# Performance work log

Hardware: AMD Instinct MI355X
Metric: run time of the kernel (lower is better)

The kernel has to match this reference:

```python
import jax, jax.numpy as jnp
import numpy as np
from jax import lax

T, B, D, H, C, G = 32, 512, 1024, 2048, 10, 16
BETA = 0.95
THRESH = 1.0


def _build_mask(key, out_f, in_f, p_intra=1.0, p_inter=0.15):
    ig, og = in_f // G, out_f // G
    same = (jnp.arange(out_f) // og)[:, None] == (jnp.arange(in_f) // ig)[None, :]
    probs = jnp.where(same, p_intra, p_inter)
    return (jax.random.uniform(key, (out_f, in_f)) < probs).astype(jnp.float32)


def setup_inputs() -> dict:
    key = jax.random.key(0)
    ks = jax.random.split(key, 12)
    def w(k, out_f, in_f):
        return jax.random.normal(k, (out_f, in_f), jnp.float32) * (1.0 / np.sqrt(in_f))
    return {
        'x_seq': jax.random.normal(ks[0], (T, B, D), jnp.float32),
        'w1': w(ks[1], H, D), 'b1': jax.random.normal(ks[2], (H,), jnp.float32) * 0.01,
        'mask1': _build_mask(ks[3], H, D),
        'w2': w(ks[4], H, H), 'b2': jax.random.normal(ks[5], (H,), jnp.float32) * 0.01,
        'mask2': _build_mask(ks[6], H, H),
        'w3': w(ks[7], H, H), 'b3': jax.random.normal(ks[8], (H,), jnp.float32) * 0.01,
        'mask3': _build_mask(ks[9], H, H),
        'w_out': w(ks[10], C, H), 'b_out': jax.random.normal(ks[11], (C,), jnp.float32) * 0.01,
    }


@jax.custom_vjp
def spike(x):
    # heaviside fire, fast_sigmoid(slope=25) surrogate gradient
    return (x > 0).astype(x.dtype)

def _spike_fwd(x):
    return spike(x), x

def _spike_bwd(x, g):
    return (g / (25.0 * jnp.abs(x) + 1.0) ** 2,)

spike.defvjp(_spike_fwd, _spike_bwd)


def _lif(cur, mem):
    # snntorch Leaky (reset-by-subtraction): reset from previous mem (detached)
    reset = lax.stop_gradient((mem > THRESH).astype(cur.dtype))
    mem = BETA * mem + cur - reset * THRESH
    spk = spike(mem - THRESH)
    return spk, mem


def reference(x_seq, w1, b1, mask1, w2, b2, mask2, w3, b3, mask3, w_out, b_out):
    # cache masked weights once (same math as per-step weight*mask)
    ew1, ew2, ew3 = w1 * mask1, w2 * mask2, w3 * mask3
    Bsz = x_seq.shape[1]
    mem1 = jnp.zeros((Bsz, H), x_seq.dtype)
    mem2 = jnp.zeros((Bsz, H), x_seq.dtype)
    mem3 = jnp.zeros((Bsz, H), x_seq.dtype)
    mem_o = jnp.zeros((Bsz, C), x_seq.dtype)
    ssum = jnp.zeros((Bsz, C), x_seq.dtype)

    def step(carry, x_t):
        mem1, mem2, mem3, mem_o, ssum = carry
        spk1, mem1 = _lif(x_t @ ew1.T + b1, mem1)
        spk2, mem2 = _lif(spk1 @ ew2.T + b2, mem2)
        spk3, mem3 = _lif(spk2 @ ew3.T + b3, mem3)
        spk_o, mem_o = _lif(spk3 @ w_out.T + b_out, mem_o)
        return (mem1, mem2, mem3, mem_o, ssum + spk_o), None

    (mem1, mem2, mem3, mem_o, ssum), _ = lax.scan(step, (mem1, mem2, mem3, mem_o, ssum), x_seq)
    return ssum
```

## Files before the change

kernel.cpp:

```cpp
#include <hip/hip_runtime.h>

#define TSTEPS 32
#define BSZ    512
#define DIN    1024
#define HID    2048
#define NCLS   10
#define BETA   0.95f
#define VTH    1.0f
#define SPKB   ((size_t)BSZ * (HID / 8))

typedef __attribute__((ext_vector_type(4))) float          f4;
typedef __attribute__((ext_vector_type(4))) float          f32x4;
typedef __attribute__((ext_vector_type(8))) __bf16         bf16x8;
typedef __attribute__((ext_vector_type(8))) unsigned short us8;
typedef __attribute__((ext_vector_type(4))) unsigned short us4;
typedef __attribute__((ext_vector_type(2))) unsigned int   u32x2;

__device__ inline unsigned short f2bf(float f) {
    unsigned u = __float_as_uint(f);
    u += 0x7FFF + ((u >> 16) & 1);
    return (unsigned short)(u >> 16);
}
__device__ inline float bf2f(unsigned short h) {
    return __uint_as_float(((unsigned)h) << 16);
}

__device__ __forceinline__ void split_f4pair(f4 v0, f4 v1, us8& o0, us8& o1, us8& o2) {
#pragma unroll
    for (int jj = 0; jj < 4; jj++) {
        float v = v0[jj];
        unsigned short h1 = f2bf(v); float r = v - bf2f(h1);
        unsigned short h2 = f2bf(r); float r2 = r - bf2f(h2);
        o0[jj] = h1; o1[jj] = h2; o2[jj] = f2bf(r2);
        v = v1[jj];
        h1 = f2bf(v); r = v - bf2f(h1);
        h2 = f2bf(r); r2 = r - bf2f(h2);
        o0[jj + 4] = h1; o1[jj + 4] = h2; o2[jj + 4] = f2bf(r2);
    }
}

__global__ __launch_bounds__(256)
void split3(const float* __restrict__ w, const float* __restrict__ m,
            unsigned short* __restrict__ h1, unsigned short* __restrict__ h2,
            unsigned short* __restrict__ h3, int n4)
{
    int i      = blockIdx.x * blockDim.x + threadIdx.x;
    int stride = gridDim.x * blockDim.x;
    for (; i < n4; i += stride) {
        f4 wv = ((const f4*)w)[i];
        f4 mv = ((const f4*)m)[i];
        us4 a, b, c;
#pragma unroll
        for (int j = 0; j < 4; j++) {
            float e  = wv[j] * mv[j];
            unsigned short x1 = f2bf(e);
            float r  = e - bf2f(x1);
            unsigned short x2 = f2bf(r);
            float r2 = r - bf2f(x2);
            a[j] = x1; b[j] = x2; c[j] = f2bf(r2);
        }
        ((us4*)h1)[i] = a;
        ((us4*)h2)[i] = b;
        ((us4*)h3)[i] = c;
    }
}

__global__ __launch_bounds__(256)
void split3q(const float* __restrict__ w, const float* __restrict__ m,
             unsigned short* __restrict__ q)
{
    const int NK = HID * HID;
    int gid = blockIdx.x * 256 + threadIdx.x;
    const int lane = gid & 63;
    const int t    = gid >> 6;
    const int kt   = t & (HID / 32 - 1);
    const int nt   = t >> 6;
    const int n = nt * 16 + (lane & 15);
    const int k = kt * 32 + (lane >> 4) * 8;
    const size_t src = (size_t)n * HID + k;
    f4 w0 = *(const f4*)(w + src),     w1v = *(const f4*)(w + src + 4);
    f4 m0 = *(const f4*)(m + src),     m1v = *(const f4*)(m + src + 4);
    us8 q0, q1, q2;
    split_f4pair(w0 * m0, w1v * m1v, q0, q1, q2);
    ((us8*)q)[gid]            = q0;
    ((us8*)(q + NK))[gid]     = q1;
    ((us8*)(q + 2 * NK))[gid] = q2;
}

__global__ __launch_bounds__(256)
void zerof(float* __restrict__ p, int n4)
{
    int i      = blockIdx.x * blockDim.x + threadIdx.x;
    int stride = gridDim.x * blockDim.x;
    f4 z = {0.f, 0.f, 0.f, 0.f};
    for (; i < n4; i += stride) ((f4*)p)[i] = z;
}

__device__ __forceinline__ void xsplit_dev(const float* __restrict__ xt,
                                           unsigned short* __restrict__ dst,
                                           int bid, int nblk, int tid)
{
    const int n4 = BSZ * DIN / 4;
    const int PS = BSZ * DIN;
    int i      = bid * 256 + tid;
    int stride = nblk * 256;
    for (; i < n4; i += stride) {
        f4 v = ((const f4*)xt)[i];
        us4 a, b, c;
#pragma unroll
        for (int j = 0; j < 4; j++) {
            float e = v[j];
            unsigned short x1 = f2bf(e);
            float r  = e - bf2f(x1);
            unsigned short x2 = f2bf(r);
            float r2 = r - bf2f(x2);
            a[j] = x1; b[j] = x2; c[j] = f2bf(r2);
        }
        ((us4*)(dst))[i]          = a;
        ((us4*)(dst + PS))[i]     = b;
        ((us4*)(dst + 2 * PS))[i] = c;
    }
}

__global__ __launch_bounds__(256)
void xsplit_k(const float* __restrict__ xt, unsigned short* __restrict__ dst)
{
    xsplit_dev(xt, dst, blockIdx.x, gridDim.x, threadIdx.x);
}

__device__ __forceinline__ void lif_epi(const f32x4 acc[2][2], const float* __restrict__ bias,
                                        float* __restrict__ memOut, unsigned char* __restrict__ sbits,
                                        int bm, int bn, int wm, int wn, int lane)
{
    const int fr = lane & 15;
#pragma unroll
    for (int fm = 0; fm < 2; fm++)
#pragma unroll
        for (int fn = 0; fn < 2; fn++) {
            const int n  = bn * 64 + wn * 32 + fn * 16 + fr;
            const float bv = bias[n];
            const int rbase = bm * 64 + wm * 32 + fm * 16 + (lane >> 4) * 4;
#pragma unroll
            for (int r = 0; r < 4; r++) {
                const int row = rbase + r;
                float* mp = memOut + (size_t)row * HID + n;
                float mo  = *mp;
                float m2  = BETA * mo + (acc[fm][fn][r] + bv) - ((mo > VTH) ? VTH : 0.f);
                *mp = m2;
                unsigned long long bal = __ballot(m2 > VTH);
                if (fr == 0) {
                    unsigned short bits = (unsigned short)(bal >> ((lane >> 4) * 16));
                    *(unsigned short*)(sbits + (size_t)row * (HID / 8) + bn * 8 + wn * 4 + fn * 2) = bits;
                }
            }
        }
}

__device__ __forceinline__ void lif_epi4b(const f32x4 (&acc)[4], const float* __restrict__ bias,
                                          float* __restrict__ memOut,
                                          unsigned char* __restrict__ sbitsOut,
                                          int bm, int bn, int wv, int lane)
{
    const int fr = lane & 15;
    const int n  = bn * 64 + wv * 16 + fr;
    const float bv = bias[n];
#pragma unroll
    for (int fm = 0; fm < 4; fm++) {
        const int rbase = bm * 64 + fm * 16 + (lane >> 4) * 4;
#pragma unroll
        for (int r = 0; r < 4; r++) {
            const int row = rbase + r;
            float* mp = memOut + (size_t)row * HID + n;
            float mo  = *mp;
            float m2  = BETA * mo + (acc[fm][r] + bv) - ((mo > VTH) ? VTH : 0.f);
            *mp = m2;
            unsigned long long bal = __ballot(m2 > VTH);
            if (fr == 0) {
                unsigned short bits = (unsigned short)(bal >> ((lane >> 4) * 16));
                *(unsigned short*)(sbitsOut + (size_t)row * (HID / 8) + bn * 8 + wv * 2) = bits;
            }
        }
    }
}

__device__ __forceinline__ void role_out_b(const unsigned char* __restrict__ sbits,
    const float* __restrict__ wo, const float* __restrict__ bo,
    float* __restrict__ memo, float* __restrict__ ssum, int b, int lane)
{
    const unsigned int bits = *(const unsigned int*)(sbits + (size_t)b * (HID / 8) + lane * 4);
    float acc[NCLS];
#pragma unroll
    for (int c = 0; c < NCLS; c++) {
        const f4* wrow = (const f4*)(wo + (size_t)c * HID + lane * 32);
        float s = 0.f;
#pragma unroll
        for (int q = 0; q < 8; q++) {
            f4 w = wrow[q];
#pragma unroll
            for (int i = 0; i < 4; i++)
                if ((bits >> (q * 4 + i)) & 1u) s += w[i];
        }
        acc[c] = s;
    }
#pragma unroll
    for (int c = 0; c < NCLS; c++)
#pragma unroll
        for (int m = 1; m < 64; m <<= 1) acc[c] += __shfl_xor(acc[c], m, 64);

    if (lane == 0) {
#pragma unroll
        for (int c = 0; c < NCLS; c++) {
            float mo  = memo[b * NCLS + c];
            float rst = (mo > VTH) ? VTH : 0.f;
            float m2  = BETA * mo + acc[c] + bo[c] - rst;
            memo[b * NCLS + c] = m2;
            if (m2 > VTH) ssum[b * NCLS + c] += 1.f;
        }
    }
}

__device__ __forceinline__ void role_l23k(unsigned char* smem,
    const unsigned char* __restrict__ sbitsIn,
    const unsigned short* __restrict__ Bq,
    const float* __restrict__ bias, float* __restrict__ memOut,
    unsigned char* __restrict__ sbitsOut, int rb, int tid)
{
    u32x2* lut = (u32x2*)smem;
    if (tid < 16) {
        u32x2 e;
        e.x = ((tid & 1) ? 0x3F80u : 0u) | ((tid & 2) ? 0x3F800000u : 0u);
        e.y = ((tid & 4) ? 0x3F80u : 0u) | ((tid & 8) ? 0x3F800000u : 0u);
        lut[tid] = e;
    }
    __syncthreads();

    const int bn = rb & 31, bm = rb >> 5;
    const int lane = tid & 63, wv = tid >> 6;
    const int fr = lane & 15, fk = (lane >> 4) * 8;

    const size_t PSQ = (size_t)HID * HID / 8;
    const us8* bP0 = (const us8*)Bq + (size_t)(bn * 4 + wv) * (HID / 32) * 64 + lane;
    const us8* bP1 = bP0 + PSQ;
    const us8* bP2 = bP1 + PSQ;

    const unsigned char* aR = sbitsIn + (size_t)(bm * 64 + fr) * (HID / 8);

    f32x4 acc[4] = {};
    us8 bb[2][3];
    us4 awq[2][4];
    us8 afP0, afP1, afP2, afP3;
    us8 afN0, afN1, afN2, afN3;

#define LDB4(SET, S) do { const int sc_ = (S) < 64 ? (S) : 63;                 \
        bb[SET][0] = bP0[sc_ * 64];                                            \
        bb[SET][1] = bP1[sc_ * 64];                                            \
        bb[SET][2] = bP2[sc_ * 64]; } while (0)

#define LDA4(SET, G) do { const int gc_ = (G) < 16 ? (G) : 15;                 \
        awq[SET][0] = *(const us4*)(aR + 0 * 16 * (HID / 8) + gc_ * 16);       \
        awq[SET][1] = *(const us4*)(aR + 1 * 16 * (HID / 8) + gc_ * 16);       \
        awq[SET][2] = *(const us4*)(aR + 2 * 16 * (HID / 8) + gc_ * 16);       \
        awq[SET][3] = *(const us4*)(aR + 3 * 16 * (HID / 8) + gc_ * 16); } while (0)

#define EXPAND(AF, W) do { unsigned by_ = ((W) >> fk) & 0xFFu;                 \
        u32x2 lo_ = lut[by_ & 15u];                                            \
        u32x2 hi_ = lut[by_ >> 4];                                             \
        ((u32x2*)&(AF))[0] = lo_;                                              \
        ((u32x2*)&(AF))[1] = hi_; } while (0)

#define EXP4(D0, D1, D2, D3, ASET, COMP) do {                                  \
        EXPAND(D0, awq[ASET][0][COMP]);                                        \
        EXPAND(D1, awq[ASET][1][COMP]);                                        \
        EXPAND(D2, awq[ASET][2][COMP]);                                        \
        EXPAND(D3, awq[ASET][3][COMP]); } while (0)

#define MM12(A0, A1, A2, A3, BSET) do {                                        \
        bf16x8 b0_ = *(const bf16x8*)&bb[BSET][0];                             \
        bf16x8 b1_ = *(const bf16x8*)&bb[BSET][1];                             \
        bf16x8 b2_ = *(const bf16x8*)&bb[BSET][2];                             \
        bf16x8 fa0_ = *(const bf16x8*)&A0;                                     \
        bf16x8 fa1_ = *(const bf16x8*)&A1;                                     \
        bf16x8 fa2_ = *(const bf16x8*)&A2;                                     \
        bf16x8 fa3_ = *(const bf16x8*)&A3;                                     \
        acc[0] = __builtin_amdgcn_mfma_f32_16x16x32_bf16(fa0_, b0_, acc[0], 0, 0, 0); \
        acc[1] = __builtin_amdgcn_mfma_f32_16x16x32_bf16(fa1_, b0_, acc[1], 0, 0, 0); \
        acc[2] = __builtin_amdgcn_mfma_f32_16x16x32_bf16(fa2_, b0_, acc[2], 0, 0, 0); \
        acc[3] = __builtin_amdgcn_mfma_f32_16x16x32_bf16(fa3_, b0_, acc[3], 0, 0, 0); \
        acc[0] = __builtin_amdgcn_mfma_f32_16x16x32_bf16(fa0_, b1_, acc[0], 0, 0, 0); \
        acc[1] = __builtin_amdgcn_mfma_f32_16x16x32_bf16(fa1_, b1_, acc[1], 0, 0, 0); \
        acc[2] = __builtin_amdgcn_mfma_f32_16x16x32_bf16(fa2_, b1_, acc[2], 0, 0, 0); \
        acc[3] = __builtin_amdgcn_mfma_f32_16x16x32_bf16(fa3_, b1_, acc[3], 0, 0, 0); \
        acc[0] = __builtin_amdgcn_mfma_f32_16x16x32_bf16(fa0_, b2_, acc[0], 0, 0, 0); \
        acc[1] = __builtin_amdgcn_mfma_f32_16x16x32_bf16(fa1_, b2_, acc[1], 0, 0, 0); \
        acc[2] = __builtin_amdgcn_mfma_f32_16x16x32_bf16(fa2_, b2_, acc[2], 0, 0, 0); \
        acc[3] = __builtin_amdgcn_mfma_f32_16x16x32_bf16(fa3_, b2_, acc[3], 0, 0, 0); \
    } while (0)

    LDB4(0, 0); LDB4(1, 1);
    LDA4(0, 0); LDA4(1, 1);
    EXP4(afP0, afP1, afP2, afP3, 0, 0);

    for (int g = 0; g < 16; g += 2) {
        const int s0 = g * 4;
        EXP4(afN0, afN1, afN2, afN3, 0, 1); MM12(afP0, afP1, afP2, afP3, 0); LDB4(0, s0 + 2);
        EXP4(afP0, afP1, afP2, afP3, 0, 2); MM12(afN0, afN1, afN2, afN3, 1); LDB4(1, s0 + 3);
        EXP4(afN0, afN1, afN2, afN3, 0, 3); MM12(afP0, afP1, afP2, afP3, 0); LDB4(0, s0 + 4);
        EXP4(afP0, afP1, afP2, afP3, 1, 0); MM12(afN0, afN1, afN2, afN3, 1); LDB4(1, s0 + 5); LDA4(0, g + 2);
        EXP4(afN0, afN1, afN2, afN3, 1, 1); MM12(afP0, afP1, afP2, afP3, 0); LDB4(0, s0 + 6);
        EXP4(afP0, afP1, afP2, afP3, 1, 2); MM12(afN0, afN1, afN2, afN3, 1); LDB4(1, s0 + 7);
        EXP4(afN0, afN1, afN2, afN3, 1, 3); MM12(afP0, afP1, afP2, afP3, 0); LDB4(0, s0 + 8);
        EXP4(afP0, afP1, afP2, afP3, 0, 0); MM12(afN0, afN1, afN2, afN3, 1); LDB4(1, s0 + 9); LDA4(1, g + 3);
    }

#undef LDB4
#undef LDA4
#undef EXPAND
#undef EXP4
#undef MM12

    lif_epi4b(acc, bias, memOut, sbitsOut, bm, bn, wv, lane);
}

__device__ __forceinline__ void role_l1s(unsigned char* smem,
    const unsigned short* __restrict__ Ap,
    const unsigned short* __restrict__ Wp,
    const float* __restrict__ bias, float* __restrict__ memOut,
    unsigned char* __restrict__ sbitsOut, int rb, int tid)
{
    auto As = reinterpret_cast<unsigned short(*)[64 * 40]>(smem);
    auto Bs = reinterpret_cast<unsigned short(*)[64 * 40]>(smem + 15360);
    const size_t APS = (size_t)BSZ * DIN;
    const size_t BPS = (size_t)HID * DIN;

    const int bn = rb & 31, bm = rb >> 5;
    const int srow = tid >> 2, skq = tid & 3;
    const int lane = tid & 63, wv = tid >> 6;
    const int wm = wv >> 1, wn = wv & 1;
    const int fr = lane & 15, fk = (lane >> 4) * 8;
    const size_t aRow = (size_t)(bm * 64 + srow) * DIN;
    const size_t bRow = (size_t)(bn * 64 + srow) * DIN;
    const int sdst = srow * 40 + skq * 8;

    f32x4 acc[2][2] = {};
    us8 aa0, aa1, aa2, bb0, bb1, bb2;

    auto ldnext = [&](int k0) {
        aa0 = *(const us8*)(Ap + aRow + k0 + skq * 8);
        aa1 = *(const us8*)(Ap + APS + aRow + k0 + skq * 8);
        aa2 = *(const us8*)(Ap + 2 * APS + aRow + k0 + skq * 8);
        bb0 = *(const us8*)(Wp + bRow + k0 + skq * 8);
        bb1 = *(const us8*)(Wp + BPS + bRow + k0 + skq * 8);
        bb2 = *(const us8*)(Wp + 2 * BPS + bRow + k0 + skq * 8);
    };
    auto stageAB = [&]() {
        *(us8*)&As[0][sdst] = aa0;
        *(us8*)&As[1][sdst] = aa1;
        *(us8*)&As[2][sdst] = aa2;
        *(us8*)&Bs[0][sdst] = bb0;
        *(us8*)&Bs[1][sdst] = bb1;
        *(us8*)&Bs[2][sdst] = bb2;
    };

    ldnext(0); stageAB();
    __syncthreads();

    const int nsteps = DIN / 32;
    for (int s = 0; s < nsteps; s++) {
        const bool more = (s + 1 < nsteps);
        if (more) ldnext((s + 1) * 32);

        bf16x8 af[3][2], bf[3][2];
#pragma unroll
        for (int p = 0; p < 3; p++)
#pragma unroll
            for (int f = 0; f < 2; f++) {
                af[p][f] = *(const bf16x8*)&As[p][(wm * 32 + f * 16 + fr) * 40 + fk];
                bf[p][f] = *(const bf16x8*)&Bs[p][(wn * 32 + f * 16 + fr) * 40 + fk];
            }
#pragma unroll
        for (int pa = 0; pa < 3; pa++)
#pragma unroll
            for (int pb = 0; pb < 3; pb++) {
                if (pa + pb <= 2) {
#pragma unroll
                    for (int fm = 0; fm < 2; fm++)
#pragma unroll
                        for (int fn = 0; fn < 2; fn++)
                            acc[fm][fn] = __builtin_amdgcn_mfma_f32_16x16x32_bf16(
                                af[pa][fm], bf[pb][fn], acc[fm][fn], 0, 0, 0);
                }
            }

        __syncthreads();
        if (more) stageAB();
        __syncthreads();
    }

    lif_epi(acc, bias, memOut, sbitsOut, bm, bn, wm, wn, lane);
}

__global__ __launch_bounds__(256, 4)
void snn_step8(const float* __restrict__ x,
               unsigned short* __restrict__ xp,
               const unsigned short* __restrict__ w1p, const float* __restrict__ b1,
               const unsigned short* __restrict__ w2q, const float* __restrict__ b2,
               const unsigned short* __restrict__ w3q, const float* __restrict__ b3,
               const float* __restrict__ wo, const float* __restrict__ bo,
               float* __restrict__ mem1, float* __restrict__ mem2, float* __restrict__ mem3,
               float* __restrict__ memo,
               unsigned char* __restrict__ spk1, unsigned char* __restrict__ spk2,
               unsigned char* __restrict__ spk3,
               float* __restrict__ ssum, int j)
{
    __shared__ __align__(16) unsigned char smem[30720];
    const int bid = blockIdx.x, tid = threadIdx.x;
    const size_t XSLOT = (size_t)3 * BSZ * DIN;

    if (bid < 256) {
        const int t = j;
        if (t <= TSTEPS - 1)
            role_l1s(smem, xp + (size_t)(t & 1) * XSLOT, w1p, b1, mem1,
                     spk1 + (size_t)(t & 1) * SPKB, bid, tid);
    } else if (bid < 512) {
        const int t = j - 1;
        if (t >= 0 && t <= TSTEPS - 1)
            role_l23k(smem, spk1 + (size_t)(t & 1) * SPKB, w2q, b2, mem2,
                      spk2 + (size_t)(t & 1) * SPKB, bid - 256, tid);
    } else if (bid < 768) {
        const int t = j - 2;
        if (t >= 0 && t <= TSTEPS - 1)
            role_l23k(smem, spk2 + (size_t)(t & 1) * SPKB, w3q, b3, mem3,
                      spk3 + (size_t)(t & 1) * SPKB, bid - 512, tid);
    } else {
        const int t1 = j + 1;
        if (t1 <= TSTEPS - 1)
            xsplit_dev(x + (size_t)t1 * BSZ * DIN,
                       xp + (size_t)(t1 & 1) * XSLOT, bid - 768, 256, tid);
        const int t = j - 3;
        if (t >= 0 && t <= TSTEPS - 1) {
            const int lane = tid & 63, wvi = tid >> 6;
            if (wvi < 2)
                role_out_b(spk3 + (size_t)(t & 1) * SPKB, wo, bo, memo, ssum,
                           (bid - 768) * 2 + wvi, lane);
        }
    }
}

extern "C" void kernel_launch(void* const* d_in, const int* in_sizes, int n_in,
                              void* d_out, int out_size, void* d_ws, size_t ws_size,
                              hipStream_t stream)
{
    const float* x  = (const float*)d_in[0];
    const float* w1 = (const float*)d_in[1];
    const float* b1 = (const float*)d_in[2];
    const float* m1 = (const float*)d_in[3];
    const float* w2 = (const float*)d_in[4];
    const float* b2 = (const float*)d_in[5];
    const float* m2 = (const float*)d_in[6];
    const float* w3 = (const float*)d_in[7];
    const float* b3 = (const float*)d_in[8];
    const float* m3 = (const float*)d_in[9];
    const float* wo = (const float*)d_in[10];
    const float* bo = (const float*)d_in[11];
    float* out = (float*)d_out;

    const size_t planeB  = (size_t)HID * HID * 2;
    const size_t plane1B = (size_t)HID * DIN * 2;
    const size_t planeXB = (size_t)BSZ * DIN * 2;
    const size_t memB    = (size_t)BSZ * HID * 4;
    const size_t memoB   = (size_t)BSZ * NCLS * 4;
    const size_t spk2B   = 2 * SPKB;

    unsigned char* base = (unsigned char*)d_ws;
    const int nW1  = HID * DIN / 4;
    const size_t HD = (size_t)HID * DIN;

    const size_t needV8 = 6 * planeB + 3 * plane1B + 6 * planeXB
                        + 3 * memB + memoB + 3 * spk2B + 4096;
    if (ws_size < needV8) return;

    unsigned short* w2q = (unsigned short*)base;
    unsigned short* w3q = (unsigned short*)(base + 3 * planeB);
    unsigned short* w1p = (unsigned short*)(base + 6 * planeB);
    unsigned short* xp  = (unsigned short*)(base + 6 * planeB + 3 * plane1B);
    unsigned char* mbase = base + 6 * planeB + 3 * plane1B + 6 * planeXB;
    float* mem1 = (float*)(mbase);
    float* mem2 = (float*)(mbase + memB);
    float* mem3 = (float*)(mbase + 2 * memB);
    float* memo = (float*)(mbase + 3 * memB);
    unsigned char* spk1 = mbase + 3 * memB + memoB;
    unsigned char* spk2 = spk1 + spk2B;
    unsigned char* spk3 = spk2 + spk2B;

    split3q<<<2048, 256, 0, stream>>>(w2, m2, w2q);
    split3q<<<2048, 256, 0, stream>>>(w3, m3, w3q);
    split3<<<1024, 256, 0, stream>>>(w1, m1, w1p, w1p + HD, w1p + 2 * HD, nW1);
    xsplit_k<<<256, 256, 0, stream>>>(x, xp);

    zerof<<<1024, 256, 0, stream>>>(mem1, (int)((3 * memB + memoB) / 16));
    zerof<<<8, 256, 0, stream>>>(out, (BSZ * NCLS) / 4);

    for (int j = 0; j <= TSTEPS + 2; j++) {
        snn_step8<<<1024, 256, 0, stream>>>(x, xp, w1p, b1, w2q, b2, w3q, b3,
                                            wo, bo, mem1, mem2, mem3, memo,
                                            spk1, spk2, spk3, out, j);
    }
}
```

Measured before the change: 1.863 ms.

## Double M tile of layer 2/3 spike GEMM blocks and remap to XCD-aware grid

Layer 2/3 blocks now compute 128 rows instead of 64 per block, with 8 accumulators per wave, so each weight fragment loaded from global memory is reused across twice as many rows, halving the B-traffic per output. Block index mapping spreads column tiles across XCDs (xcd + pg*8), the grid shrinks from 1024 to 768 blocks, and launch bounds drop to 3 waves-per-SIMD occupancy to fit the larger register footprint. The A-fragment expansion pipeline is simplified (no separate prefetched expanded registers), which may expose more LUT latency; fewer blocks per layer also reduces parallelism.

```diff
diff --git a/kernel.cpp b/kernel.cpp
--- a/kernel.cpp
+++ b/kernel.cpp
@@ -156,7 +156,7 @@
         }
 }
 
-__device__ __forceinline__ void lif_epi4b(const f32x4 (&acc)[4], const float* __restrict__ bias,
+__device__ __forceinline__ void lif_epi8b(const f32x4 (&acc)[8], const float* __restrict__ bias,
                                           float* __restrict__ memOut,
                                           unsigned char* __restrict__ sbitsOut,
                                           int bm, int bn, int wv, int lane)
@@ -165,8 +165,8 @@
     const int n  = bn * 64 + wv * 16 + fr;
     const float bv = bias[n];
 #pragma unroll
-    for (int fm = 0; fm < 4; fm++) {
-        const int rbase = bm * 64 + fm * 16 + (lane >> 4) * 4;
+    for (int fm = 0; fm < 8; fm++) {
+        const int rbase = bm * 128 + fm * 16 + (lane >> 4) * 4;
 #pragma unroll
         for (int r = 0; r < 4; r++) {
             const int row = rbase + r;
@@ -219,11 +219,11 @@
     }
 }
 
-__device__ __forceinline__ void role_l23k(unsigned char* smem,
+__device__ __forceinline__ void role_l23m(unsigned char* smem,
     const unsigned char* __restrict__ sbitsIn,
     const unsigned short* __restrict__ Bq,
     const float* __restrict__ bias, float* __restrict__ memOut,
-    unsigned char* __restrict__ sbitsOut, int rb, int tid)
+    unsigned char* __restrict__ sbitsOut, int g, int tid)
 {
     u32x2* lut = (u32x2*)smem;
     if (tid < 16) {
@@ -234,7 +234,9 @@
     }
     __syncthreads();
 
-    const int bn = rb & 31, bm = rb >> 5;
+    const int xcd = g & 7, pg = (g >> 3) & 3, bm = g >> 5;
+    const int bn  = xcd + pg * 8;
+
     const int lane = tid & 63, wv = tid >> 6;
     const int fr = lane & 15, fk = (lane >> 4) * 8;
 
@@ -243,24 +245,26 @@
     const us8* bP1 = bP0 + PSQ;
     const us8* bP2 = bP1 + PSQ;
 
-    const unsigned char* aR = sbitsIn + (size_t)(bm * 64 + fr) * (HID / 8);
-
-    f32x4 acc[4] = {};
+    const unsigned char* aR = sbitsIn + (size_t)(bm * 128 + fr) * (HID / 8);
+
+    f32x4 acc[8] = {};
     us8 bb[2][3];
-    us4 awq[2][4];
-    us8 afP0, afP1, afP2, afP3;
-    us8 afN0, afN1, afN2, afN3;
+    us4 awq[2][8];
 
 #define LDB4(SET, S) do { const int sc_ = (S) < 64 ? (S) : 63;                 \
         bb[SET][0] = bP0[sc_ * 64];                                            \
         bb[SET][1] = bP1[sc_ * 64];                                            \
         bb[SET][2] = bP2[sc_ * 64]; } while (0)
 
-#define LDA4(SET, G) do { const int gc_ = (G) < 16 ? (G) : 15;                 \
+#define LDA8(SET, G) do { const int gc_ = (G) < 16 ? (G) : 15;                 \
         awq[SET][0] = *(const us4*)(aR + 0 * 16 * (HID / 8) + gc_ * 16);       \
         awq[SET][1] = *(const us4*)(aR + 1 * 16 * (HID / 8) + gc_ * 16);       \
         awq[SET][2] = *(const us4*)(aR + 2 * 16 * (HID / 8) + gc_ * 16);       \
-        awq[SET][3] = *(const us4*)(aR + 3 * 16 * (HID / 8) + gc_ * 16); } while (0)
+        awq[SET][3] = *(const us4*)(aR + 3 * 16 * (HID / 8) + gc_ * 16);       \
+        awq[SET][4] = *(const us4*)(aR + 4 * 16 * (HID / 8) + gc_ * 16);       \
+        awq[SET][5] = *(const us4*)(aR + 5 * 16 * (HID / 8) + gc_ * 16);       \
+        awq[SET][6] = *(const us4*)(aR + 6 * 16 * (HID / 8) + gc_ * 16);       \
+        awq[SET][7] = *(const us4*)(aR + 7 * 16 * (HID / 8) + gc_ * 16); } while (0)
 
 #define EXPAND(AF, W) do { unsigned by_ = ((W) >> fk) & 0xFFu;                 \
         u32x2 lo_ = lut[by_ & 15u];                                            \
@@ -268,57 +272,55 @@
         ((u32x2*)&(AF))[0] = lo_;                                              \
         ((u32x2*)&(AF))[1] = hi_; } while (0)
 
-#define EXP4(D0, D1, D2, D3, ASET, COMP) do {                                  \
-        EXPAND(D0, awq[ASET][0][COMP]);                                        \
-        EXPAND(D1, awq[ASET][1][COMP]);                                        \
-        EXPAND(D2, awq[ASET][2][COMP]);                                        \
-        EXPAND(D3, awq[ASET][3][COMP]); } while (0)
-
-#define MM12(A0, A1, A2, A3, BSET) do {                                        \
+#define MMQ(AX, IDX) do {                                                      \
+        bf16x8 fa_ = *(const bf16x8*)&AX;                                      \
+        acc[IDX] = __builtin_amdgcn_mfma_f32_16x16x32_bf16(fa_, b0_, acc[IDX], 0, 0, 0); \
+        acc[IDX] = __builtin_amdgcn_mfma_f32_16x16x32_bf16(fa_, b1_, acc[IDX], 0, 0, 0); \
+        acc[IDX] = __builtin_amdgcn_mfma_f32_16x16x32_bf16(fa_, b2_, acc[IDX], 0, 0, 0); \
+    } while (0)
+
+#define STEP(BSET, ASET, COMP) do {                                            \
         bf16x8 b0_ = *(const bf16x8*)&bb[BSET][0];                             \
         bf16x8 b1_ = *(const bf16x8*)&bb[BSET][1];                             \
         bf16x8 b2_ = *(const bf16x8*)&bb[BSET][2];                             \
-        bf16x8 fa0_ = *(const bf16x8*)&A0;                                     \
-        bf16x8 fa1_ = *(const bf16x8*)&A1;                                     \
-        bf16x8 fa2_ = *(const bf16x8*)&A2;                                     \
-        bf16x8 fa3_ = *(const bf16x8*)&A3;                                     \
-        acc[0] = __builtin_amdgcn_mfma_f32_16x16x32_bf16(fa0_, b0_, acc[0], 0, 0, 0); \
-        acc[1] = __builtin_amdgcn_mfma_f32_16x16x32_bf16(fa1_, b0_, acc[1], 0, 0, 0); \
-        acc[2] = __builtin_amdgcn_mfma_f32_16x16x32_bf16(fa2_, b0_, acc[2], 0, 0, 0); \
-        acc[3] = __builtin_amdgcn_mfma_f32_16x16x32_bf16(fa3_, b0_, acc[3], 0, 0, 0); \
-        acc[0] = __builtin_amdgcn_mfma_f32_16x16x32_bf16(fa0_, b1_, acc[0], 0, 0, 0); \
-        acc[1] = __builtin_amdgcn_mfma_f32_16x16x32_bf16(fa1_, b1_, acc[1], 0, 0, 0); \
-        acc[2] = __builtin_amdgcn_mfma_f32_16x16x32_bf16(fa2_, b1_, acc[2], 0, 0, 0); \
-        acc[3] = __builtin_amdgcn_mfma_f32_16x16x32_bf16(fa3_, b1_, acc[3], 0, 0, 0); \
-        acc[0] = __builtin_amdgcn_mfma_f32_16x16x32_bf16(fa0_, b2_, acc[0], 0, 0, 0); \
-        acc[1] = __builtin_amdgcn_mfma_f32_16x16x32_bf16(fa1_, b2_, acc[1], 0, 0, 0); \
-        acc[2] = __builtin_amdgcn_mfma_f32_16x16x32_bf16(fa2_, b2_, acc[2], 0, 0, 0); \
-        acc[3] = __builtin_amdgcn_mfma_f32_16x16x32_bf16(fa3_, b2_, acc[3], 0, 0, 0); \
+        us8 a0_, a1_, a2_, a3_;                                                \
+        EXPAND(a0_, awq[ASET][0][COMP]);                                       \
+        EXPAND(a1_, awq[ASET][1][COMP]);                                       \
+        EXPAND(a2_, awq[ASET][2][COMP]);                                       \
+        EXPAND(a3_, awq[ASET][3][COMP]);                                       \
+        MMQ(a0_, 0); MMQ(a1_, 1); MMQ(a2_, 2); MMQ(a3_, 3);                    \
+        us8 a4_, a5_, a6_, a7_;                                                \
+        EXPAND(a4_, awq[ASET][4][COMP]);                                       \
+        EXPAND(a5_, awq[ASET][5][COMP]);                                       \
+        EXPAND(a6_, awq[ASET][6][COMP]);                                       \
+        EXPAND(a7_, awq[ASET][7][COMP]);                                       \
+        MMQ(a4_, 4); MMQ(a5_, 5); MMQ(a6_, 6); MMQ(a7_, 7);                    \
     } while (0)
 
     LDB4(0, 0); LDB4(1, 1);
-    LDA4(0, 0); LDA4(1, 1);
-    EXP4(afP0, afP1, afP2, afP3, 0, 0);
-
-    for (int g = 0; g < 16; g += 2) {
-        const int s0 = g * 4;
-        EXP4(afN0, afN1, afN2, afN3, 0, 1); MM12(afP0, afP1, afP2, afP3, 0); LDB4(0, s0 + 2);
-        EXP4(afP0, afP1, afP2, afP3, 0, 2); MM12(afN0, afN1, afN2, afN3, 1); LDB4(1, s0 + 3);
-        EXP4(afN0, afN1, afN2, afN3, 0, 3); MM12(afP0, afP1, afP2, afP3, 0); LDB4(0, s0 + 4);
-        EXP4(afP0, afP1, afP2, afP3, 1, 0); MM12(afN0, afN1, afN2, afN3, 1); LDB4(1, s0 + 5); LDA4(0, g + 2);
-        EXP4(afN0, afN1, afN2, afN3, 1, 1); MM12(afP0, afP1, afP2, afP3, 0); LDB4(0, s0 + 6);
-        EXP4(afP0, afP1, afP2, afP3, 1, 2); MM12(afN0, afN1, afN2, afN3, 1); LDB4(1, s0 + 7);
-        EXP4(afN0, afN1, afN2, afN3, 1, 3); MM12(afP0, afP1, afP2, afP3, 0); LDB4(0, s0 + 8);
-        EXP4(afP0, afP1, afP2, afP3, 0, 0); MM12(afN0, afN1, afN2, afN3, 1); LDB4(1, s0 + 9); LDA4(1, g + 3);
+    LDA8(0, 0); LDA8(1, 1);
+
+    for (int gg = 0; gg < 16; gg += 2) {
+        const int s0 = gg * 4;
+        STEP(0, 0, 0); LDB4(0, s0 + 2);
+        STEP(1, 0, 1); LDB4(1, s0 + 3);
+        STEP(0, 0, 2); LDB4(0, s0 + 4);
+        STEP(1, 0, 3); LDB4(1, s0 + 5);
+        LDA8(0, gg + 2);
+        STEP(0, 1, 0); LDB4(0, s0 + 6);
+        STEP(1, 1, 1); LDB4(1, s0 + 7);
+        STEP(0, 1, 2); LDB4(0, s0 + 8);
+        STEP(1, 1, 3); LDB4(1, s0 + 9);
+        LDA8(1, gg + 3);
     }
 
 #undef LDB4
-#undef LDA4
+#undef LDA8
 #undef EXPAND
-#undef EXP4
-#undef MM12
-
-    lif_epi4b(acc, bias, memOut, sbitsOut, bm, bn, wv, lane);
+#undef MMQ
+#undef STEP
+
+    lif_epi8b(acc, bias, memOut, sbitsOut, bm, bn, wv, lane);
 }
 
 __device__ __forceinline__ void role_l1s(unsigned char* smem,
@@ -399,8 +401,8 @@
     lif_epi(acc, bias, memOut, sbitsOut, bm, bn, wm, wn, lane);
 }
 
-__global__ __launch_bounds__(256, 4)
-void snn_step8(const float* __restrict__ x,
+__global__ __launch_bounds__(256, 3)
+void snn_step9(const float* __restrict__ x,
                unsigned short* __restrict__ xp,
                const unsigned short* __restrict__ w1p, const float* __restrict__ b1,
                const unsigned short* __restrict__ w2q, const float* __restrict__ b2,
@@ -421,27 +423,27 @@
         if (t <= TSTEPS - 1)
             role_l1s(smem, xp + (size_t)(t & 1) * XSLOT, w1p, b1, mem1,
                      spk1 + (size_t)(t & 1) * SPKB, bid, tid);
-    } else if (bid < 512) {
+    } else if (bid < 384) {
         const int t = j - 1;
         if (t >= 0 && t <= TSTEPS - 1)
-            role_l23k(smem, spk1 + (size_t)(t & 1) * SPKB, w2q, b2, mem2,
+            role_l23m(smem, spk1 + (size_t)(t & 1) * SPKB, w2q, b2, mem2,
                       spk2 + (size_t)(t & 1) * SPKB, bid - 256, tid);
-    } else if (bid < 768) {
+    } else if (bid < 512) {
         const int t = j - 2;
         if (t >= 0 && t <= TSTEPS - 1)
-            role_l23k(smem, spk2 + (size_t)(t & 1) * SPKB, w3q, b3, mem3,
-                      spk3 + (size_t)(t & 1) * SPKB, bid - 512, tid);
+            role_l23m(smem, spk2 + (size_t)(t & 1) * SPKB, w3q, b3, mem3,
+                      spk3 + (size_t)(t & 1) * SPKB, bid - 384, tid);
     } else {
         const int t1 = j + 1;
         if (t1 <= TSTEPS - 1)
             xsplit_dev(x + (size_t)t1 * BSZ * DIN,
-                       xp + (size_t)(t1 & 1) * XSLOT, bid - 768, 256, tid);
+                       xp + (size_t)(t1 & 1) * XSLOT, bid - 512, 256, tid);
         const int t = j - 3;
         if (t >= 0 && t <= TSTEPS - 1) {
             const int lane = tid & 63, wvi = tid >> 6;
             if (wvi < 2)
                 role_out_b(spk3 + (size_t)(t & 1) * SPKB, wo, bo, memo, ssum,
-                           (bid - 768) * 2 + wvi, lane);
+                           (bid - 512) * 2 + wvi, lane);
         }
     }
 }
@@ -475,9 +477,9 @@
     const int nW1  = HID * DIN / 4;
     const size_t HD = (size_t)HID * DIN;
 
-    const size_t needV8 = 6 * planeB + 3 * plane1B + 6 * planeXB
+    const size_t needV9 = 6 * planeB + 3 * plane1B + 6 * planeXB
                         + 3 * memB + memoB + 3 * spk2B + 4096;
-    if (ws_size < needV8) return;
+    if (ws_size < needV9) return;
 
     unsigned short* w2q = (unsigned short*)base;
     unsigned short* w3q = (unsigned short*)(base + 3 * planeB);
@@ -501,8 +503,8 @@
     zerof<<<8, 256, 0, stream>>>(out, (BSZ * NCLS) / 4);
 
     for (int j = 0; j <= TSTEPS + 2; j++) {
-        snn_step8<<<1024, 256, 0, stream>>>(x, xp, w1p, b1, w2q, b2, w3q, b3,
-                                            wo, bo, mem1, mem2, mem3, memo,
-                                            spk1, spk2, spk3, out, j);
-    }
-}
+        snn_step9<<<768, 256, 0, stream>>>(x, xp, w1p, b1, w2q, b2, w3q, b3,
+                                           wo, bo, mem1, mem2, mem3, memo,
+                                           spk1, spk2, spk3, out, j);
+    }
+}
```

Result: slower. 2.263 ms (+21.5%).

## Retile layer 2/3 blocks to 128x32 with 2x2 wave grid, drop expand pipelining

Applied to the files above, without the earlier changes.

Changes the per-block tile of the hidden-layer matmuls from 64 rows x 64 columns (four waves splitting columns) to 128 rows x 32 columns, with waves arranged as 2 row groups by 2 column groups. Each wave still computes a 64x16 output tile, but the block now reuses each weight column strip across two row groups rather than each spike row strip across four column groups. This shifts the block's reuse from spike bits toward weights and changes cache traffic. The software-pipelined spike-bit expansion (ping-pong A fragments) is also replaced by expanding inline before each MFMA group. That simplifies the code and may lower register pressure, but it exposes the LDS lookup latency before the MFMAs.

```diff
diff --git a/kernel.cpp b/kernel.cpp
--- a/kernel.cpp
+++ b/kernel.cpp
@@ -156,17 +156,17 @@
         }
 }
 
-__device__ __forceinline__ void lif_epi4b(const f32x4 (&acc)[4], const float* __restrict__ bias,
+__device__ __forceinline__ void lif_epi4c(const f32x4 (&acc)[4], const float* __restrict__ bias,
                                           float* __restrict__ memOut,
                                           unsigned char* __restrict__ sbitsOut,
-                                          int bm, int bn, int wv, int lane)
+                                          int rowBase, int colBase, int lane)
 {
     const int fr = lane & 15;
-    const int n  = bn * 64 + wv * 16 + fr;
+    const int n  = colBase + fr;
     const float bv = bias[n];
 #pragma unroll
     for (int fm = 0; fm < 4; fm++) {
-        const int rbase = bm * 64 + fm * 16 + (lane >> 4) * 4;
+        const int rbase = rowBase + fm * 16 + (lane >> 4) * 4;
 #pragma unroll
         for (int r = 0; r < 4; r++) {
             const int row = rbase + r;
@@ -177,7 +177,7 @@
             unsigned long long bal = __ballot(m2 > VTH);
             if (fr == 0) {
                 unsigned short bits = (unsigned short)(bal >> ((lane >> 4) * 16));
-                *(unsigned short*)(sbitsOut + (size_t)row * (HID / 8) + bn * 8 + wv * 2) = bits;
+                *(unsigned short*)(sbitsOut + (size_t)row * (HID / 8) + (colBase >> 3)) = bits;
             }
         }
     }
@@ -219,7 +219,7 @@
     }
 }
 
-__device__ __forceinline__ void role_l23k(unsigned char* smem,
+__device__ __forceinline__ void role_l23p(unsigned char* smem,
     const unsigned char* __restrict__ sbitsIn,
     const unsigned short* __restrict__ Bq,
     const float* __restrict__ bias, float* __restrict__ memOut,
@@ -234,22 +234,22 @@
     }
     __syncthreads();
 
-    const int bn = rb & 31, bm = rb >> 5;
+    const int bn = rb & 63, bm = rb >> 6;
     const int lane = tid & 63, wv = tid >> 6;
+    const int rg = wv >> 1, cg = wv & 1;
     const int fr = lane & 15, fk = (lane >> 4) * 8;
 
-    const size_t PSQ = (size_t)HID * HID / 8;
-    const us8* bP0 = (const us8*)Bq + (size_t)(bn * 4 + wv) * (HID / 32) * 64 + lane;
-    const us8* bP1 = bP0 + PSQ;
-    const us8* bP2 = bP1 + PSQ;
-
-    const unsigned char* aR = sbitsIn + (size_t)(bm * 64 + fr) * (HID / 8);
+    const int nt = bn * 2 + cg;
+    const us8* bP0 = (const us8*)Bq + (size_t)nt * (HID / 32) * 64 + lane;
+    const us8* bP1 = bP0 + (size_t)HID * HID / 8;
+    const us8* bP2 = bP1 + (size_t)HID * HID / 8;
+
+    const int rowBase = bm * 128 + rg * 64;
+    const unsigned char* aR = sbitsIn + (size_t)(rowBase + fr) * (HID / 8);
 
     f32x4 acc[4] = {};
     us8 bb[2][3];
     us4 awq[2][4];
-    us8 afP0, afP1, afP2, afP3;
-    us8 afN0, afN1, afN2, afN3;
 
 #define LDB4(SET, S) do { const int sc_ = (S) < 64 ? (S) : 63;                 \
         bb[SET][0] = bP0[sc_ * 64];                                            \
@@ -268,57 +268,56 @@
         ((u32x2*)&(AF))[0] = lo_;                                              \
         ((u32x2*)&(AF))[1] = hi_; } while (0)
 
-#define EXP4(D0, D1, D2, D3, ASET, COMP) do {                                  \
-        EXPAND(D0, awq[ASET][0][COMP]);                                        \
-        EXPAND(D1, awq[ASET][1][COMP]);                                        \
-        EXPAND(D2, awq[ASET][2][COMP]);                                        \
-        EXPAND(D3, awq[ASET][3][COMP]); } while (0)
-
-#define MM12(A0, A1, A2, A3, BSET) do {                                        \
+#define STEP(BSET, ASET, COMP) do {                                            \
+        us8 a0_, a1_, a2_, a3_;                                                \
+        EXPAND(a0_, awq[ASET][0][COMP]);                                       \
+        EXPAND(a1_, awq[ASET][1][COMP]);                                       \
+        EXPAND(a2_, awq[ASET][2][COMP]);                                       \
+        EXPAND(a3_, awq[ASET][3][COMP]);                                       \
         bf16x8 b0_ = *(const bf16x8*)&bb[BSET][0];                             \
         bf16x8 b1_ = *(const bf16x8*)&bb[BSET][1];                             \
         bf16x8 b2_ = *(const bf16x8*)&bb[BSET][2];                             \
-        bf16x8 fa0_ = *(const bf16x8*)&A0;                                     \
-        bf16x8 fa1_ = *(const bf16x8*)&A1;                                     \
-        bf16x8 fa2_ = *(const bf16x8*)&A2;                                     \
-        bf16x8 fa3_ = *(const bf16x8*)&A3;                                     \
+        bf16x8 fa0_ = *(const bf16x8*)&a0_;                                    \
+        bf16x8 fa1_ = *(const bf16x8*)&a1_;                                    \
+        bf16x8 fa2_ = *(const bf16x8*)&a2_;                                    \
+        bf16x8 fa3_ = *(const bf16x8*)&a3_;                                    \
         acc[0] = __builtin_amdgcn_mfma_f32_16x16x32_bf16(fa0_, b0_, acc[0], 0, 0, 0); \
+        acc[0] = __builtin_amdgcn_mfma_f32_16x16x32_bf16(fa0_, b1_, acc[0], 0, 0, 0); \
+        acc[0] = __builtin_amdgcn_mfma_f32_16x16x32_bf16(fa0_, b2_, acc[0], 0, 0, 0); \
         acc[1] = __builtin_amdgcn_mfma_f32_16x16x32_bf16(fa1_, b0_, acc[1], 0, 0, 0); \
+        acc[1] = __builtin_amdgcn_mfma_f32_16x16x32_bf16(fa1_, b1_, acc[1], 0, 0, 0); \
+        acc[1] = __builtin_amdgcn_mfma_f32_16x16x32_bf16(fa1_, b2_, acc[1], 0, 0, 0); \
         acc[2] = __builtin_amdgcn_mfma_f32_16x16x32_bf16(fa2_, b0_, acc[2], 0, 0, 0); \
+        acc[2] = __builtin_amdgcn_mfma_f32_16x16x32_bf16(fa2_, b1_, acc[2], 0, 0, 0); \
+        acc[2] = __builtin_amdgcn_mfma_f32_16x16x32_bf16(fa2_, b2_, acc[2], 0, 0, 0); \
         acc[3] = __builtin_amdgcn_mfma_f32_16x16x32_bf16(fa3_, b0_, acc[3], 0, 0, 0); \
-        acc[0] = __builtin_amdgcn_mfma_f32_16x16x32_bf16(fa0_, b1_, acc[0], 0, 0, 0); \
-        acc[1] = __builtin_amdgcn_mfma_f32_16x16x32_bf16(fa1_, b1_, acc[1], 0, 0, 0); \
-        acc[2] = __builtin_amdgcn_mfma_f32_16x16x32_bf16(fa2_, b1_, acc[2], 0, 0, 0); \
         acc[3] = __builtin_amdgcn_mfma_f32_16x16x32_bf16(fa3_, b1_, acc[3], 0, 0, 0); \
-        acc[0] = __builtin_amdgcn_mfma_f32_16x16x32_bf16(fa0_, b2_, acc[0], 0, 0, 0); \
-        acc[1] = __builtin_amdgcn_mfma_f32_16x16x32_bf16(fa1_, b2_, acc[1], 0, 0, 0); \
-        acc[2] = __builtin_amdgcn_mfma_f32_16x16x32_bf16(fa2_, b2_, acc[2], 0, 0, 0); \
         acc[3] = __builtin_amdgcn_mfma_f32_16x16x32_bf16(fa3_, b2_, acc[3], 0, 0, 0); \
     } while (0)
 
     LDB4(0, 0); LDB4(1, 1);
     LDA4(0, 0); LDA4(1, 1);
-    EXP4(afP0, afP1, afP2, afP3, 0, 0);
 
     for (int g = 0; g < 16; g += 2) {
         const int s0 = g * 4;
-        EXP4(afN0, afN1, afN2, afN3, 0, 1); MM12(afP0, afP1, afP2, afP3, 0); LDB4(0, s0 + 2);
-        EXP4(afP0, afP1, afP2, afP3, 0, 2); MM12(afN0, afN1, afN2, afN3, 1); LDB4(1, s0 + 3);
-        EXP4(afN0, afN1, afN2, afN3, 0, 3); MM12(afP0, afP1, afP2, afP3, 0); LDB4(0, s0 + 4);
-        EXP4(afP0, afP1, afP2, afP3, 1, 0); MM12(afN0, afN1, afN2, afN3, 1); LDB4(1, s0 + 5); LDA4(0, g + 2);
-        EXP4(afN0, afN1, afN2, afN3, 1, 1); MM12(afP0, afP1, afP2, afP3, 0); LDB4(0, s0 + 6);
-        EXP4(afP0, afP1, afP2, afP3, 1, 2); MM12(afN0, afN1, afN2, afN3, 1); LDB4(1, s0 + 7);
-        EXP4(afN0, afN1, afN2, afN3, 1, 3); MM12(afP0, afP1, afP2, afP3, 0); LDB4(0, s0 + 8);
-        EXP4(afP0, afP1, afP2, afP3, 0, 0); MM12(afN0, afN1, afN2, afN3, 1); LDB4(1, s0 + 9); LDA4(1, g + 3);
+        STEP(0, 0, 0); LDB4(0, s0 + 2);
+        STEP(1, 0, 1); LDB4(1, s0 + 3);
+        STEP(0, 0, 2); LDB4(0, s0 + 4);
+        STEP(1, 0, 3); LDB4(1, s0 + 5);
+        LDA4(0, g + 2);
+        STEP(0, 1, 0); LDB4(0, s0 + 6);
+        STEP(1, 1, 1); LDB4(1, s0 + 7);
+        STEP(0, 1, 2); LDB4(0, s0 + 8);
+        STEP(1, 1, 3); LDB4(1, s0 + 9);
+        LDA4(1, g + 3);
     }
 
 #undef LDB4
 #undef LDA4
 #undef EXPAND
-#undef EXP4
-#undef MM12
-
-    lif_epi4b(acc, bias, memOut, sbitsOut, bm, bn, wv, lane);
+#undef STEP
+
+    lif_epi4c(acc, bias, memOut, sbitsOut, rowBase, bn * 32 + cg * 16, lane);
 }
 
 __device__ __forceinline__ void role_l1s(unsigned char* smem,
@@ -400,17 +399,17 @@
 }
 
 __global__ __launch_bounds__(256, 4)
-void snn_step8(const float* __restrict__ x,
-               unsigned short* __restrict__ xp,
-               const unsigned short* __restrict__ w1p, const float* __restrict__ b1,
-               const unsigned short* __restrict__ w2q, const float* __restrict__ b2,
-               const unsigned short* __restrict__ w3q, const float* __restrict__ b3,
-               const float* __restrict__ wo, const float* __restrict__ bo,
-               float* __restrict__ mem1, float* __restrict__ mem2, float* __restrict__ mem3,
-               float* __restrict__ memo,
-               unsigned char* __restrict__ spk1, unsigned char* __restrict__ spk2,
-               unsigned char* __restrict__ spk3,
-               float* __restrict__ ssum, int j)
+void snn_step10(const float* __restrict__ x,
+                unsigned short* __restrict__ xp,
+                const unsigned short* __restrict__ w1p, const float* __restrict__ b1,
+                const unsigned short* __restrict__ w2q, const float* __restrict__ b2,
+                const unsigned short* __restrict__ w3q, const float* __restrict__ b3,
+                const float* __restrict__ wo, const float* __restrict__ bo,
+                float* __restrict__ mem1, float* __restrict__ mem2, float* __restrict__ mem3,
+                float* __restrict__ memo,
+                unsigned char* __restrict__ spk1, unsigned char* __restrict__ spk2,
+                unsigned char* __restrict__ spk3,
+                float* __restrict__ ssum, int j)
 {
     __shared__ __align__(16) unsigned char smem[30720];
     const int bid = blockIdx.x, tid = threadIdx.x;
@@ -424,12 +423,12 @@
     } else if (bid < 512) {
         const int t = j - 1;
         if (t >= 0 && t <= TSTEPS - 1)
-            role_l23k(smem, spk1 + (size_t)(t & 1) * SPKB, w2q, b2, mem2,
+            role_l23p(smem, spk1 + (size_t)(t & 1) * SPKB, w2q, b2, mem2,
                       spk2 + (size_t)(t & 1) * SPKB, bid - 256, tid);
     } else if (bid < 768) {
         const int t = j - 2;
         if (t >= 0 && t <= TSTEPS - 1)
-            role_l23k(smem, spk2 + (size_t)(t & 1) * SPKB, w3q, b3, mem3,
+            role_l23p(smem, spk2 + (size_t)(t & 1) * SPKB, w3q, b3, mem3,
                       spk3 + (size_t)(t & 1) * SPKB, bid - 512, tid);
     } else {
         const int t1 = j + 1;
@@ -475,9 +474,9 @@
     const int nW1  = HID * DIN / 4;
     const size_t HD = (size_t)HID * DIN;
 
-    const size_t needV8 = 6 * planeB + 3 * plane1B + 6 * planeXB
-                        + 3 * memB + memoB + 3 * spk2B + 4096;
-    if (ws_size < needV8) return;
+    const size_t needV10 = 6 * planeB + 3 * plane1B + 6 * planeXB
+                         + 3 * memB + memoB + 3 * spk2B + 4096;
+    if (ws_size < needV10) return;
 
     unsigned short* w2q = (unsigned short*)base;
     unsigned short* w3q = (unsigned short*)(base + 3 * planeB);
@@ -501,8 +500,8 @@
     zerof<<<8, 256, 0, stream>>>(out, (BSZ * NCLS) / 4);
 
     for (int j = 0; j <= TSTEPS + 2; j++) {
-        snn_step8<<<1024, 256, 0, stream>>>(x, xp, w1p, b1, w2q, b2, w3q, b3,
-                                            wo, bo, mem1, mem2, mem3, memo,
-                                            spk1, spk2, spk3, out, j);
-    }
-}
+        snn_step10<<<1024, 256, 0, stream>>>(x, xp, w1p, b1, w2q, b2, w3q, b3,
+                                             wo, bo, mem1, mem2, mem3, memo,
+                                             spk1, spk2, spk3, out, j);
+    }
+}
```

New measurement: 1.740 ms, median of 2. 1.07x faster.
